# Kernel optimization log

Hardware: AMD Instinct MI355X
Metric: run time of the kernel (lower is better)

Reference implementation:

```python
import jax, jax.numpy as jnp
import numpy as np
from math import factorial

# irreps as (mul, l, parity): hidden = 64x0e + 32x1o + 16x2e (dim 240), edge = 1x0e + 1x1o (dim 4)
HIDDEN = [(64, 0, 1), (32, 1, -1), (16, 2, 1)]
EDGE = [(1, 0, 1), (1, 1, -1)]
N_LAYERS = 6
N_NODES = 10000
N_EDGES = 160000
N_GRAPHS = 64
IN_DIM = 3
LATENT = 128  # config.LATENT_DIM_GNN
W_STD = 0.1   # weight scale keeps 6 residual bilinear layers numerically stable

def _dim(ir):
    return sum(m * (2 * l + 1) for m, l, _ in ir)

def _slices(ir):
    out, o = [], 0
    for m, l, _ in ir:
        d = m * (2 * l + 1)
        out.append(slice(o, o + d))
        o += d
    return out

def _cg(j1, m1, j2, m2, j3, m3):
    # Condon-Shortley Clebsch-Gordan <j1 m1 j2 m2 | j3 m3> (Racah formula)
    if m1 + m2 != m3:
        return 0.0
    f = lambda n: float(factorial(n))
    pre = ((2 * j3 + 1) * f(j3 + j1 - j2) * f(j3 - j1 + j2) * f(j1 + j2 - j3) / f(j1 + j2 + j3 + 1)) ** 0.5
    pre *= (f(j3 + m3) * f(j3 - m3) * f(j1 - m1) * f(j1 + m1) * f(j2 - m2) * f(j2 + m2)) ** 0.5
    s = 0.0
    for k in range(j1 + j2 - j3 + 1):
        a = [k, j1 + j2 - j3 - k, j1 - m1 - k, j2 + m2 - k, j3 - j2 + m1 + k, j3 - j1 - m2 + k]
        if any(t < 0 for t in a):
            continue
        s += (-1) ** k / np.prod([f(t) for t in a])
    return pre * s

def _w3j_complex(l1, l2, l3):
    W = np.zeros((2 * l1 + 1, 2 * l2 + 1, 2 * l3 + 1))
    for m1 in range(-l1, l1 + 1):
        for m2 in range(-l2, l2 + 1):
            m3 = -(m1 + m2)
            if abs(m3) > l3:
                continue
            W[m1 + l1, m2 + l2, m3 + l3] = (-1) ** (l1 - l2 - m3) / np.sqrt(2 * l3 + 1) * _cg(l1, m1, l2, m2, l3, -m3)
    return W

def _A_real(l):
    # real SH in terms of complex SH: Y^r_m = sum_mu A[m, mu] Y_mu
    A = np.zeros((2 * l + 1, 2 * l + 1), dtype=complex)
    A[l, l] = 1.0
    for m in range(1, l + 1):
        A[l + m, l + m] = (-1) ** m / np.sqrt(2)
        A[l + m, l - m] = 1 / np.sqrt(2)
        A[l - m, l + m] = -1j * (-1) ** m / np.sqrt(2)
        A[l - m, l - m] = 1j / np.sqrt(2)
    return A

_W3J_CACHE = {}
def real_w3j(l1, l2, l3):
    key = (l1, l2, l3)
    if key not in _W3J_CACHE:
        T = np.einsum('ad,be,cf,def->abc', _A_real(l1), _A_real(l2), _A_real(l3), _w3j_complex(l1, l2, l3).astype(complex))
        T = np.real(T)  # exactly real when l1+l2+l3 is even (true for all paths here)
        _W3J_CACHE[key] = (T / np.linalg.norm(T)).astype(np.float32)
    return _W3J_CACHE[key]

def _paths(ir1, ir2, irout):
    ps = []
    for i1, (_, l1, p1) in enumerate(ir1):
        for i2, (_, l2, p2) in enumerate(ir2):
            for i3, (_, l3, p3) in enumerate(irout):
                if p3 == p1 * p2 and abs(l1 - l2) <= l3 <= l1 + l2:
                    ps.append((i1, i2, i3))
    return ps

MSG_PATHS = _paths(HIDDEN, EDGE, HIDDEN)
UPD_PATHS = _paths(HIDDEN, HIDDEN, HIDDEN)

def _tp_wsize(ir1, ir2, irout, paths):
    return sum(ir1[a][0] * ir2[b][0] * irout[c][0] for a, b, c in paths)

MSG_WSIZE = _tp_wsize(HIDDEN, EDGE, HIDDEN, MSG_PATHS)
UPD_WSIZE = _tp_wsize(HIDDEN, HIDDEN, HIDDEN, UPD_PATHS)
LIN_WSIZE = sum(m * m for m, _, _ in HIDDEN)

def tensor_product(x1, x2, w_flat, ir1, ir2, irout, paths):
    # FullyConnectedTensorProduct: per-path CG-coupled bilinear op with path normalization
    s1, s2, s3 = _slices(ir1), _slices(ir2), _slices(irout)
    npo = [0] * len(irout)
    for _, _, i3 in paths:
        npo[i3] += 1
    out = jnp.zeros((x1.shape[0], _dim(irout)), dtype=x1.dtype)
    off = 0
    for i1, i2, i3 in paths:
        m1, l1, _ = ir1[i1]; m2, l2, _ = ir2[i2]; m3, l3, _ = irout[i3]
        W = w_flat[off:off + m1 * m2 * m3].reshape(m1, m2, m3)
        off += m1 * m2 * m3
        C = jnp.asarray(real_w3j(l1, l2, l3), dtype=x1.dtype)
        a = x1[:, s1[i1]].reshape(-1, m1, 2 * l1 + 1)
        b = x2[:, s2[i2]].reshape(-1, m2, 2 * l2 + 1)
        alpha = 1.0 / np.sqrt(m1 * m2 * npo[i3])
        y = alpha * jnp.einsum('nui,nvj,uvw,ijk->nwk', a, b, W, C)
        out = out.at[:, s3[i3]].add(y.reshape(-1, m3 * (2 * l3 + 1)))
    return out

def irreps_linear(x, w_flat, ir):
    # e3nn Linear with identical in/out irreps: per-irrep mixing of multiplicities
    sl = _slices(ir)
    parts, off = [], 0
    for i, (m, l, _) in enumerate(ir):
        W = w_flat[off:off + m * m].reshape(m, m)
        off += m * m
        xi = x[:, sl[i]].reshape(-1, m, 2 * l + 1)
        parts.append((jnp.einsum('nui,uv->nvi', xi, W) / np.sqrt(m)).reshape(-1, m * (2 * l + 1)))
    return jnp.concatenate(parts, axis=-1)

def _forward(x, pos, w_init, w_tp_msg, w_lin_msg, w_tp_upd, w_lin_upd, w_final, edge_index, batch):
    row, col = edge_index[0], edge_index[1]
    r_vec = pos[row] - pos[col]                           # (E, 3)
    dist = jnp.linalg.norm(r_vec, axis=-1, keepdims=True)
    nvec = r_vec / jnp.maximum(dist, 1e-8)
    edge_attr = jnp.concatenate([dist, nvec], axis=-1)    # layer consumes [dist, r_vec] = 1x0e + 1x1o
    h = jnp.zeros((x.shape[0], _dim(HIDDEN)), dtype=x.dtype)
    h = h.at[:, :64].set(x @ w_init / np.sqrt(IN_DIM))    # initial Linear hits only 0e channels
    for L in range(N_LAYERS):
        hj = h[col]  # gather neighbor (source) features
        msg = tensor_product(hj, edge_attr, w_tp_msg[L], HIDDEN, EDGE, HIDDEN, MSG_PATHS) \
            + irreps_linear(hj, w_lin_msg[L], HIDDEN)
        agg = jax.ops.segment_sum(msg, row, num_segments=N_NODES)  # scatter-add aggregate
        upd = tensor_product(h, agg, w_tp_upd[L], HIDDEN, HIDDEN, HIDDEN, UPD_PATHS) \
            + irreps_linear(h, w_lin_upd[L], HIDDEN)
        h = h + upd  # residual
    scal = h[:, :64]  # 0e (invariant) channels
    cnt = jax.ops.segment_sum(jnp.ones((x.shape[0],), x.dtype), batch, num_segments=N_GRAPHS)
    pooled = jax.ops.segment_sum(scal, batch, num_segments=N_GRAPHS) / jnp.maximum(cnt, 1.0)[:, None]
    return pooled @ w_final / np.sqrt(64)

def setup_inputs() -> dict:
    key = jax.random.key(0)
    ks = jax.random.split(key, 10)
    return {
        'x': jax.random.normal(ks[0], (N_NODES, IN_DIM), jnp.float32),
        'pos': jax.random.normal(ks[1], (N_NODES, 3), jnp.float32),
        'w_init': jax.random.normal(ks[2], (IN_DIM, 64), jnp.float32),
        'w_tp_msg': jax.random.normal(ks[3], (N_LAYERS, MSG_WSIZE), jnp.float32) * W_STD,
        'w_lin_msg': jax.random.normal(ks[4], (N_LAYERS, LIN_WSIZE), jnp.float32) * W_STD,
        'w_tp_upd': jax.random.normal(ks[5], (N_LAYERS, UPD_WSIZE), jnp.float32) * W_STD,
        'w_lin_upd': jax.random.normal(ks[6], (N_LAYERS, LIN_WSIZE), jnp.float32) * W_STD,
        'w_final': jax.random.normal(ks[7], (64, LATENT), jnp.float32),
        'edge_index': jax.random.randint(ks[8], (2, N_EDGES), 0, N_NODES),
        'batch': jnp.sort(jax.random.randint(ks[9], (N_NODES,), 0, N_GRAPHS)),
    }

def reference(x, pos, w_init, w_tp_msg, w_lin_msg, w_tp_upd, w_lin_upd, w_final, edge_index, batch):
    return _forward(x, pos, w_init, w_tp_msg, w_lin_msg, w_tp_upd, w_lin_upd, w_final, edge_index, batch)
```

## Files before the change

kernel.cpp:

```cpp
#include <hip/hip_runtime.h>
#include <cmath>
#include <cstring>
#include <complex>

#define NN 10000
#define NE 160000
#define HD 240
#define ZD 912
#define NG 64
#define MSG_WS 10496
#define UPD_WS 561152
#define LIN_WS 5376

struct CMsgPre { float a000, a011, a110, a112, a211; float c101[9]; float c202[25]; };
struct CEdge   { float c011[9]; float c110[9]; float c112[45]; float c211[45]; };
struct CUpdS   { float s000; float c011[9]; float c022[25]; float c101[9]; float c202[25]; };
struct CUpdD   { float c110[9]; float c220[25]; };
struct CUpdP   { float c112[45]; float c121[45]; float c211[45]; float c222[125]; };


__global__ __launch_bounds__(256) void k_edge_attr(
    const float* __restrict__ pos, const int* __restrict__ ei, CEdge C,
    float* __restrict__ EA, float* __restrict__ CN) {
  int e = blockIdx.x * 256 + threadIdx.x;
  if (e >= NE) return;
  int r = ei[e], c = ei[NE + e];
  float dx = pos[r*3+0] - pos[c*3+0];
  float dy = pos[r*3+1] - pos[c*3+1];
  float dz = pos[r*3+2] - pos[c*3+2];
  float d = sqrtf(dx*dx + dy*dy + dz*dz);
  float inv = 1.0f / fmaxf(d, 1e-8f);
  float n0 = dx*inv, n1 = dy*inv, n2 = dz*inv;
  EA[e*4+0] = d; EA[e*4+1] = n0; EA[e*4+2] = n1; EA[e*4+3] = n2;
  float* cn = CN + (size_t)e*36;
#pragma unroll
  for (int k = 0; k < 3; k++)
    cn[k] = n0*C.c011[0*3+k] + n1*C.c011[1*3+k] + n2*C.c011[2*3+k];
#pragma unroll
  for (int i = 0; i < 3; i++)
    cn[3+i] = n0*C.c110[i*3+0] + n1*C.c110[i*3+1] + n2*C.c110[i*3+2];
#pragma unroll
  for (int i = 0; i < 3; i++)
#pragma unroll
    for (int k = 0; k < 5; k++)
      cn[6+i*5+k] = n0*C.c112[(i*3+0)*5+k] + n1*C.c112[(i*3+1)*5+k] + n2*C.c112[(i*3+2)*5+k];
#pragma unroll
  for (int i = 0; i < 5; i++)
#pragma unroll
    for (int k = 0; k < 3; k++)
      cn[21+i*3+k] = n0*C.c211[(i*3+0)*3+k] + n1*C.c211[(i*3+1)*3+k] + n2*C.c211[(i*3+2)*3+k];
}

__global__ __launch_bounds__(256) void k_h_init(
    const float* __restrict__ x, const float* __restrict__ wi, float* __restrict__ HT) {
  int n = blockIdx.x * 256 + threadIdx.x;
  int e = blockIdx.y;
  if (n >= NN) return;
  float v = 0.f;
  if (e < 64)
    v = (x[n*3+0]*wi[0*64+e] + x[n*3+1]*wi[64+e] + x[n*3+2]*wi[128+e]) * 0.57735026918962576f;
  HT[e*NN + n] = v;
}

__global__ __launch_bounds__(256) void k_node_pre(
    const float* __restrict__ HT, const float* __restrict__ Wm, const float* __restrict__ Wl,
    CMsgPre C, float* __restrict__ Z) {
  int n = blockIdx.x * 256 + threadIdx.x;
  int widx = blockIdx.y;
  if (n >= NN) return;
  float acc = 0.f;
  if (widx < 64) {
    int w = widx;
    for (int u = 0; u < 64; u++) acc += HT[u*NN+n] * Wm[u*64+w];
    acc *= C.a000;
  } else if (widx < 96) {
    int w = widx - 64;
    for (int u = 0; u < 64; u++) acc += HT[u*NN+n] * Wm[4096 + u*32+w];
    acc *= C.a011;
  } else if (widx < 192) {
    int t = widx - 96, w = t/3, k = t - w*3;
    for (int u = 0; u < 32; u++) {
      float g = HT[(64+u*3+0)*NN+n]*C.c101[0*3+k]
              + HT[(64+u*3+1)*NN+n]*C.c101[1*3+k]
              + HT[(64+u*3+2)*NN+n]*C.c101[2*3+k];
      acc += Wm[6144 + u*32+w] * g;
    }
  } else if (widx < 384) {
    int t = widx - 192, w = t/3, i = t - w*3;
    for (int u = 0; u < 32; u++) acc += HT[(64+u*3+i)*NN+n] * Wm[7168 + u*64+w];
    acc *= C.a110;
  } else if (widx < 432) {
    int t = widx - 384, w = t/3, i = t - w*3;
    for (int u = 0; u < 32; u++) acc += HT[(64+u*3+i)*NN+n] * Wm[9216 + u*16+w];
    acc *= C.a112;
  } else if (widx < 512) {
    int t = widx - 432, w = t/5, k = t - w*5;
    for (int u = 0; u < 16; u++) {
      float g = 0.f;
#pragma unroll
      for (int i = 0; i < 5; i++) g += HT[(160+u*5+i)*NN+n] * C.c202[i*5+k];
      acc += Wm[9728 + u*16+w] * g;
    }
  } else if (widx < 672) {
    int t = widx - 512, w = t/5, i = t - w*5;
    for (int u = 0; u < 16; u++) acc += HT[(160+u*5+i)*NN+n] * Wm[9984 + u*32+w];
    acc *= C.a211;
  } else {
    int e2 = widx - 672;
    if (e2 < 64) {
      for (int u = 0; u < 64; u++) acc += HT[u*NN+n] * Wl[u*64+e2];
      acc *= 0.125f;
    } else if (e2 < 160) {
      int t = e2 - 64, v = t/3, i = t - v*3;
      for (int u = 0; u < 32; u++) acc += HT[(64+u*3+i)*NN+n] * Wl[4096 + u*32+v];
      acc *= 0.17677669529663687f;
    } else {
      int t = e2 - 160, v = t/5, i = t - v*5;
      for (int u = 0; u < 16; u++) acc += HT[(160+u*5+i)*NN+n] * Wl[5120 + u*16+v];
      acc *= 0.25f;
    }
  }
  Z[(size_t)n*ZD + widx] = acc;
}

__global__ __launch_bounds__(256) void k_edge(
    const int* __restrict__ ei, const float* __restrict__ EA, const float* __restrict__ CN,
    const float* __restrict__ Z, float* __restrict__ AGG) {
  __shared__ float zsh[4][ZD];
  int lane = threadIdx.x & 63, wid = threadIdx.x >> 6;
  int wg = blockIdx.x * 4 + wid;
  int stride = gridDim.x * 4;
  int iters = (NE + stride - 1) / stride;
  for (int it = 0; it < iters; ++it) {
    int e = wg + it * stride;
    bool act = e < NE;
    int r = 0;
    float s = 0.f;
    const float* cn = CN;
    if (act) {
      r = ei[e];
      int c = ei[NE + e];
      s = EA[e*4];
      cn = CN + (size_t)e*36;
      const float* zr = Z + (size_t)c*ZD;
      for (int t = lane; t < ZD; t += 64) zsh[wid][t] = zr[t];
    }
    __syncthreads();
    if (act) {
      const float* z = zsh[wid];
#pragma unroll
      for (int j = 0; j < 4; j++) {
        int idx = lane + 64*j;
        if (idx < HD) {
          float y = z[672 + idx];
          if (idx < 64) {
            int w = idx;
            y += s * z[w];
#pragma unroll
            for (int i = 0; i < 3; i++) y += z[192 + w*3 + i] * cn[3+i];
          } else if (idx < 160) {
            int t = idx - 64, w = t/3, k = t - w*3;
            y += cn[k] * z[64 + w] + s * z[96 + t];
#pragma unroll
            for (int i = 0; i < 5; i++) y += z[512 + w*5 + i] * cn[21 + i*3 + k];
          } else {
            int t = idx - 160, w = t/5, k = t - w*5;
            y += s * z[432 + t];
#pragma unroll
            for (int i = 0; i < 3; i++) y += z[384 + w*3 + i] * cn[6 + i*5 + k];
          }
          atomicAdd(&AGG[(size_t)r*HD + idx], y);
        }
      }
    }
    __syncthreads();
  }
}

__global__ __launch_bounds__(256) void k_transpose(
    const float* __restrict__ A_nm, float* __restrict__ A_t) {
  int n = blockIdx.x * 256 + threadIdx.x;
  int e = blockIdx.y;
  if (n >= NN) return;
  A_t[e*NN + n] = A_nm[(size_t)n*HD + e];
}

__global__ __launch_bounds__(256) void k_upd(
    const float* __restrict__ A,
    const float* __restrict__ B,
    const float* __restrict__ W,
    CUpdS CS, CUpdD CD, CUpdP CP,
    float* __restrict__ UPD) {
  __shared__ float lds[4096];
  int tid = threadIdx.x;
  int n = blockIdx.x * 256 + tid;
  bool act = n < NN;
  int nc = act ? n : NN - 1;
  int py = blockIdx.y;

  if (py < 4) {
    int w0 = py * 16;
    float y[16];
#pragma unroll
    for (int w = 0; w < 16; w++) y[w] = 0.f;

    for (int c = 0; c < 16; ++c) {
      __syncthreads();
      for (int t = tid; t < 4096; t += 256) {
        int u2 = t >> 10, v = (t >> 4) & 63, w = t & 15;
        lds[t] = W[(((c << 2) + u2) * 64 + v) * 64 + w0 + w];
      }
      __syncthreads();
      float ha[4];
#pragma unroll
      for (int u2 = 0; u2 < 4; u2++) ha[u2] = A[((c << 2) + u2) * NN + nc] * CS.s000;
#pragma unroll 2
      for (int v = 0; v < 64; ++v) {
        float bv = B[v * NN + nc];
#pragma unroll
        for (int u2 = 0; u2 < 4; u2++) {
          float p = ha[u2] * bv;
          const float* wl = lds + (u2 << 10) + (v << 4);
#pragma unroll
          for (int w = 0; w < 16; w++) y[w] += p * wl[w];
        }
      }
    }

    for (int c = 0; c < 4; ++c) {
      __syncthreads();
      for (int t = tid; t < 4096; t += 256) {
        int u2 = t >> 9, v = (t >> 4) & 31, w = t & 15;
        lds[t] = W[409600 + ((c * 8 + u2) * 32 + v) * 64 + w0 + w];
      }
      __syncthreads();
      float a[8][3];
#pragma unroll
      for (int u2 = 0; u2 < 8; u2++)
#pragma unroll
        for (int i = 0; i < 3; i++) a[u2][i] = A[(64 + (c * 8 + u2) * 3 + i) * NN + nc];
#pragma unroll 2
      for (int v = 0; v < 32; ++v) {
        float b0 = B[(64 + v * 3 + 0) * NN + nc], b1 = B[(64 + v * 3 + 1) * NN + nc],
              b2 = B[(64 + v * 3 + 2) * NN + nc];
        float bt[3];
#pragma unroll
        for (int i = 0; i < 3; i++)
          bt[i] = CD.c110[i * 3 + 0] * b0 + CD.c110[i * 3 + 1] * b1 + CD.c110[i * 3 + 2] * b2;
#pragma unroll
        for (int u2 = 0; u2 < 8; u2++) {
          float D = a[u2][0] * bt[0] + a[u2][1] * bt[1] + a[u2][2] * bt[2];
          const float* wl = lds + u2 * 512 + v * 16;
#pragma unroll
          for (int w = 0; w < 16; w++) y[w] += D * wl[w];
        }
      }
    }

    __syncthreads();
    for (int t = tid; t < 4096; t += 256) {
      int u = t >> 8, v = (t >> 4) & 15, w = t & 15;
      lds[t] = W[540672 + (u * 16 + v) * 64 + w0 + w];
    }
    __syncthreads();
    for (int ug = 0; ug < 2; ++ug) {
      float a[8][5];
#pragma unroll
      for (int u2 = 0; u2 < 8; u2++)
#pragma unroll
        for (int i = 0; i < 5; i++) a[u2][i] = A[(160 + (ug * 8 + u2) * 5 + i) * NN + nc];
      for (int v = 0; v < 16; ++v) {
        float b[5];
#pragma unroll
        for (int j = 0; j < 5; j++) b[j] = B[(160 + v * 5 + j) * NN + nc];
        float bt[5];
#pragma unroll
        for (int i = 0; i < 5; i++) {
          float t2 = 0.f;
#pragma unroll
          for (int j = 0; j < 5; j++) t2 += CD.c220[i * 5 + j] * b[j];
          bt[i] = t2;
        }
#pragma unroll
        for (int u2 = 0; u2 < 8; u2++) {
          float D = 0.f;
#pragma unroll
          for (int i = 0; i < 5; i++) D += a[u2][i] * bt[i];
          const float* wl = lds + (ug * 8 + u2) * 256 + v * 16;
#pragma unroll
          for (int w = 0; w < 16; w++) y[w] += D * wl[w];
        }
      }
    }

    if (act) {
#pragma unroll
      for (int w = 0; w < 16; w++) UPD[(w0 + w) * NN + nc] = y[w];
    }

  } else if (py < 8) {
    int w0 = (py - 4) * 8;
    float y[24];
#pragma unroll
    for (int q = 0; q < 24; q++) y[q] = 0.f;

    for (int c = 0; c < 4; ++c) {
      __syncthreads();
      for (int t = tid; t < 4096; t += 256) {
        int u2 = t >> 8, v = (t >> 3) & 31, w = t & 7;
        lds[t] = W[262144 + ((c * 16 + u2) * 32 + v) * 32 + w0 + w];
      }
      __syncthreads();
      float a[16];
#pragma unroll
      for (int u2 = 0; u2 < 16; u2++) a[u2] = A[(c * 16 + u2) * NN + nc];
#pragma unroll 2
      for (int v = 0; v < 32; ++v) {
        float b0 = B[(64 + v * 3 + 0) * NN + nc], b1 = B[(64 + v * 3 + 1) * NN + nc],
              b2 = B[(64 + v * 3 + 2) * NN + nc];
        float bc[3];
#pragma unroll
        for (int k = 0; k < 3; k++) bc[k] = b0 * CS.c011[k] + b1 * CS.c011[3 + k] + b2 * CS.c011[6 + k];
        float g8[8];
#pragma unroll
        for (int w = 0; w < 8; w++) g8[w] = 0.f;
#pragma unroll
        for (int u2 = 0; u2 < 16; u2++) {
          const float* wl = lds + u2 * 256 + v * 8;
#pragma unroll
          for (int w = 0; w < 8; w++) g8[w] += a[u2] * wl[w];
        }
#pragma unroll
        for (int w = 0; w < 8; w++)
#pragma unroll
          for (int k = 0; k < 3; k++) y[w * 3 + k] += bc[k] * g8[w];
      }
    }

    for (int c = 0; c < 4; ++c) {
      __syncthreads();
      for (int t = tid; t < 4096; t += 256) {
        int u2 = t >> 9, v = (t >> 3) & 63, w = t & 7;
        lds[t] = W[344064 + ((c * 8 + u2) * 64 + v) * 32 + w0 + w];
      }
      __syncthreads();
      float ac[8][3];
#pragma unroll
      for (int u2 = 0; u2 < 8; u2++) {
        float a0 = A[(64 + (c * 8 + u2) * 3 + 0) * NN + nc];
        float a1 = A[(64 + (c * 8 + u2) * 3 + 1) * NN + nc];
        float a2 = A[(64 + (c * 8 + u2) * 3 + 2) * NN + nc];
#pragma unroll
        for (int k = 0; k < 3; k++)
          ac[u2][k] = a0 * CS.c101[k] + a1 * CS.c101[3 + k] + a2 * CS.c101[6 + k];
      }
      float g[8][8];
#pragma unroll
      for (int u2 = 0; u2 < 8; u2++)
#pragma unroll
        for (int w = 0; w < 8; w++) g[u2][w] = 0.f;
#pragma unroll 2
      for (int v = 0; v < 64; ++v) {
        float bv = B[v * NN + nc];
#pragma unroll
        for (int u2 = 0; u2 < 8; u2++) {
          const float* wl = lds + u2 * 512 + v * 8;
#pragma unroll
          for (int w = 0; w < 8; w++) g[u2][w] += bv * wl[w];
        }
      }
#pragma unroll
      for (int u2 = 0; u2 < 8; u2++)
#pragma unroll
        for (int w = 0; w < 8; w++)
#pragma unroll
          for (int k = 0; k < 3; k++) y[w * 3 + k] += ac[u2][k] * g[u2][w];
    }

    __syncthreads();
    for (int t = tid; t < 4096; t += 256) {
      int u = t >> 7, v = (t >> 3) & 15, w = t & 7;
      lds[t] = W[491520 + (u * 16 + v) * 32 + w0 + w];
    }
    __syncthreads();
    for (int ug = 0; ug < 4; ++ug) {
      float a[8][3];
#pragma unroll
      for (int u2 = 0; u2 < 8; u2++)
#pragma unroll
        for (int i = 0; i < 3; i++) a[u2][i] = A[(64 + (ug * 8 + u2) * 3 + i) * NN + nc];
      for (int v = 0; v < 16; ++v) {
        float b[5];
#pragma unroll
        for (int j = 0; j < 5; j++) b[j] = B[(160 + v * 5 + j) * NN + nc];
        float bt[9];
#pragma unroll
        for (int i = 0; i < 3; i++)
#pragma unroll
          for (int k = 0; k < 3; k++) {
            float t2 = 0.f;
#pragma unroll
            for (int j = 0; j < 5; j++) t2 += b[j] * CP.c121[(i * 5 + j) * 3 + k];
            bt[i * 3 + k] = t2;
          }
#pragma unroll
        for (int u2 = 0; u2 < 8; u2++) {
          float P[3];
#pragma unroll
          for (int k = 0; k < 3; k++)
            P[k] = a[u2][0] * bt[k] + a[u2][1] * bt[3 + k] + a[u2][2] * bt[6 + k];
          const float* wl = lds + (ug * 8 + u2) * 128 + v * 8;
#pragma unroll
          for (int w = 0; w < 8; w++)
#pragma unroll
            for (int k = 0; k < 3; k++) y[w * 3 + k] += P[k] * wl[w];
        }
      }
    }

    __syncthreads();
    for (int t = tid; t < 4096; t += 256) {
      int u = t >> 8, v = (t >> 3) & 31, w = t & 7;
      lds[t] = W[524288 + (u * 32 + v) * 32 + w0 + w];
    }
    __syncthreads();
    for (int ug = 0; ug < 2; ++ug) {
      float a[8][5];
#pragma unroll
      for (int u2 = 0; u2 < 8; u2++)
#pragma unroll
        for (int i = 0; i < 5; i++) a[u2][i] = A[(160 + (ug * 8 + u2) * 5 + i) * NN + nc];
#pragma unroll 2
      for (int v = 0; v < 32; ++v) {
        float b0 = B[(64 + v * 3 + 0) * NN + nc], b1 = B[(64 + v * 3 + 1) * NN + nc],
              b2 = B[(64 + v * 3 + 2) * NN + nc];
        float bt[15];
#pragma unroll
        for (int i = 0; i < 5; i++)
#pragma unroll
          for (int k = 0; k < 3; k++)
            bt[i * 3 + k] = b0 * CP.c211[(i * 3 + 0) * 3 + k] + b1 * CP.c211[(i * 3 + 1) * 3 + k] +
                            b2 * CP.c211[(i * 3 + 2) * 3 + k];
#pragma unroll
        for (int u2 = 0; u2 < 8; u2++) {
          float P[3];
#pragma unroll
          for (int k = 0; k < 3; k++) {
            float t2 = 0.f;
#pragma unroll
            for (int i = 0; i < 5; i++) t2 += a[u2][i] * bt[i * 3 + k];
            P[k] = t2;
          }
          const float* wl = lds + (ug * 8 + u2) * 256 + v * 8;
#pragma unroll
          for (int w = 0; w < 8; w++)
#pragma unroll
            for (int k = 0; k < 3; k++) y[w * 3 + k] += P[k] * wl[w];
        }
      }
    }

    if (act) {
#pragma unroll
      for (int w = 0; w < 8; w++)
#pragma unroll
        for (int k = 0; k < 3; k++) UPD[(64 + (w0 + w) * 3 + k) * NN + nc] = y[w * 3 + k];
    }

  } else {
    int w0 = (py - 8) * 4;
    float y[20];
#pragma unroll
    for (int q = 0; q < 20; q++) y[q] = 0.f;

    __syncthreads();
    for (int t = tid; t < 4096; t += 256) {
      int u = t >> 6, v = (t >> 2) & 15, w = t & 3;
      lds[t] = W[327680 + (u * 16 + v) * 16 + w0 + w];
    }
    __syncthreads();
    for (int ug = 0; ug < 4; ++ug) {
      float a[16];
#pragma unroll
      for (int u2 = 0; u2 < 16; u2++) a[u2] = A[(ug * 16 + u2) * NN + nc];
      for (int v = 0; v < 16; ++v) {
        float b[5];
#pragma unroll
        for (int j = 0; j < 5; j++) b[j] = B[(160 + v * 5 + j) * NN + nc];
        float bc[5];
#pragma unroll
        for (int k = 0; k < 5; k++) {
          float t2 = 0.f;
#pragma unroll
          for (int j = 0; j < 5; j++) t2 += b[j] * CS.c022[j * 5 + k];
          bc[k] = t2;
        }
        float g4[4];
#pragma unroll
        for (int w = 0; w < 4; w++) g4[w] = 0.f;
#pragma unroll
        for (int u2 = 0; u2 < 16; u2++) {
          const float* wl = lds + (ug * 16 + u2) * 64 + v * 4;
#pragma unroll
          for (int w = 0; w < 4; w++) g4[w] += a[u2] * wl[w];
        }
#pragma unroll
        for (int w = 0; w < 4; w++)
#pragma unroll
          for (int k = 0; k < 5; k++) y[w * 5 + k] += bc[k] * g4[w];
      }
    }

    __syncthreads();
    for (int t = tid; t < 4096; t += 256) {
      int u = t >> 8, v = (t >> 2) & 63, w = t & 3;
      lds[t] = W[507904 + (u * 64 + v) * 16 + w0 + w];
    }
    __syncthreads();
    for (int ug = 0; ug < 2; ++ug) {
      float ac[8][5];
#pragma unroll
      for (int u2 = 0; u2 < 8; u2++) {
        float a[5];
#pragma unroll
        for (int i = 0; i < 5; i++) a[i] = A[(160 + (ug * 8 + u2) * 5 + i) * NN + nc];
#pragma unroll
        for (int k = 0; k < 5; k++) {
          float t2 = 0.f;
#pragma unroll
          for (int i = 0; i < 5; i++) t2 += a[i] * CS.c202[i * 5 + k];
          ac[u2][k] = t2;
        }
      }
      float g[8][4];
#pragma unroll
      for (int u2 = 0; u2 < 8; u2++)
#pragma unroll
        for (int w = 0; w < 4; w++) g[u2][w] = 0.f;
#pragma unroll 2
      for (int v = 0; v < 64; ++v) {
        float bv = B[v * NN + nc];
#pragma unroll
        for (int u2 = 0; u2 < 8; u2++) {
          const float* wl = lds + (ug * 8 + u2) * 256 + v * 4;
#pragma unroll
          for (int w = 0; w < 4; w++) g[u2][w] += bv * wl[w];
        }
      }
#pragma unroll
      for (int u2 = 0; u2 < 8; u2++)
#pragma unroll
        for (int w = 0; w < 4; w++)
#pragma unroll
          for (int k = 0; k < 5; k++) y[w * 5 + k] += ac[u2][k] * g[u2][w];
    }

    __syncthreads();
    for (int t = tid; t < 4096; t += 256) {
      int u = t >> 7, v = (t >> 2) & 31, w = t & 3;
      lds[t] = W[475136 + (u * 32 + v) * 16 + w0 + w];
    }
    __syncthreads();
    for (int ug = 0; ug < 4; ++ug) {
      float a[8][3];
#pragma unroll
      for (int u2 = 0; u2 < 8; u2++)
#pragma unroll
        for (int i = 0; i < 3; i++) a[u2][i] = A[(64 + (ug * 8 + u2) * 3 + i) * NN + nc];
#pragma unroll 2
      for (int v = 0; v < 32; ++v) {
        float b0 = B[(64 + v * 3 + 0) * NN + nc], b1 = B[(64 + v * 3 + 1) * NN + nc],
              b2 = B[(64 + v * 3 + 2) * NN + nc];
        float bt[15];
#pragma unroll
        for (int i = 0; i < 3; i++)
#pragma unroll
          for (int k = 0; k < 5; k++)
            bt[i * 5 + k] = b0 * CP.c112[(i * 3 + 0) * 5 + k] + b1 * CP.c112[(i * 3 + 1) * 5 + k] +
                            b2 * CP.c112[(i * 3 + 2) * 5 + k];
#pragma unroll
        for (int u2 = 0; u2 < 8; u2++) {
          float P[5];
#pragma unroll
          for (int k = 0; k < 5; k++)
            P[k] = a[u2][0] * bt[k] + a[u2][1] * bt[5 + k] + a[u2][2] * bt[10 + k];
          const float* wl = lds + ((ug * 8 + u2) * 32 + v) * 4;
#pragma unroll
          for (int w = 0; w < 4; w++)
#pragma unroll
            for (int k = 0; k < 5; k++) y[w * 5 + k] += P[k] * wl[w];
        }
      }
    }

    __syncthreads();
    for (int t = tid; t < 1024; t += 256) {
      int u = t >> 6, v = (t >> 2) & 15, w = t & 3;
      lds[t] = W[557056 + (u * 16 + v) * 16 + w0 + w];
    }
    __syncthreads();
    for (int ug = 0; ug < 2; ++ug) {
      float a[8][5];
#pragma unroll
      for (int u2 = 0; u2 < 8; u2++)
#pragma unroll
        for (int i = 0; i < 5; i++) a[u2][i] = A[(160 + (ug * 8 + u2) * 5 + i) * NN + nc];
      for (int v = 0; v < 16; ++v) {
        float b[5];
#pragma unroll
        for (int j = 0; j < 5; j++) b[j] = B[(160 + v * 5 + j) * NN + nc];
        float bt[25];
#pragma unroll
        for (int i = 0; i < 5; i++)
#pragma unroll
          for (int k = 0; k < 5; k++) {
            float t2 = 0.f;
#pragma unroll
            for (int j = 0; j < 5; j++) t2 += b[j] * CP.c222[(i * 5 + j) * 5 + k];
            bt[i * 5 + k] = t2;
          }
#pragma unroll
        for (int u2 = 0; u2 < 8; u2++) {
          float P[5];
#pragma unroll
          for (int k = 0; k < 5; k++) {
            float t2 = 0.f;
#pragma unroll
            for (int i = 0; i < 5; i++) t2 += a[u2][i] * bt[i * 5 + k];
            P[k] = t2;
          }
          const float* wl = lds + (ug * 8 + u2) * 64 + v * 4;
#pragma unroll
          for (int w = 0; w < 4; w++)
#pragma unroll
            for (int k = 0; k < 5; k++) y[w * 5 + k] += P[k] * wl[w];
        }
      }
    }

    if (act) {
#pragma unroll
      for (int w = 0; w < 4; w++)
#pragma unroll
        for (int k = 0; k < 5; k++) UPD[(160 + (w0 + w) * 5 + k) * NN + nc] = y[w * 5 + k];
    }
  }
}

__global__ __launch_bounds__(256) void k_apply(
    const float* __restrict__ Hsrc, const float* __restrict__ UPD,
    const float* __restrict__ Wl, float* __restrict__ Hdst) {
  int n = blockIdx.x * 256 + threadIdx.x;
  int e = blockIdx.y;
  if (n >= NN) return;
  float lin = 0.f;
  if (e < 64) {
    for (int u = 0; u < 64; u++) lin += Hsrc[u*NN+n] * Wl[u*64+e];
    lin *= 0.125f;
  } else if (e < 160) {
    int t = e - 64, v = t/3, i = t - v*3;
    for (int u = 0; u < 32; u++) lin += Hsrc[(64+u*3+i)*NN+n] * Wl[4096 + u*32+v];
    lin *= 0.17677669529663687f;
  } else {
    int t = e - 160, v = t/5, i = t - v*5;
    for (int u = 0; u < 16; u++) lin += Hsrc[(160+u*5+i)*NN+n] * Wl[5120 + u*16+v];
    lin *= 0.25f;
  }
  Hdst[e*NN + n] = Hsrc[e*NN + n] + UPD[e*NN + n] + lin;
}

__global__ __launch_bounds__(256) void k_cnt(const int* __restrict__ batch, float* __restrict__ CNT) {
  int n = blockIdx.x * 256 + threadIdx.x;
  if (n >= NN) return;
  atomicAdd(&CNT[batch[n]], 1.0f);
}

__global__ __launch_bounds__(256) void k_pool(
    const float* __restrict__ HT, const int* __restrict__ batch, float* __restrict__ POOL) {
  int n = blockIdx.x * 256 + threadIdx.x;
  int w = blockIdx.y;
  if (n >= NN) return;
  atomicAdd(&POOL[batch[n]*64 + w], HT[w*NN + n]);
}

__global__ __launch_bounds__(256) void k_out(
    const float* __restrict__ POOL, const float* __restrict__ CNT,
    const float* __restrict__ wf, float* __restrict__ out) {
  int tid = blockIdx.x * 256 + threadIdx.x;
  if (tid >= NG * 128) return;
  int g = tid >> 7, d = tid & 127;
  float inv = 1.0f / fmaxf(CNT[g], 1.0f);
  float acc = 0.f;
  for (int w = 0; w < 64; w++) acc += POOL[g*64 + w] * wf[w*128 + d];
  out[tid] = acc * inv * 0.125f;
}

typedef std::complex<double> cd;
static double hfact(int nn) { double f = 1; for (int i = 2; i <= nn; i++) f *= i; return f; }
static double hcg(int j1,int m1,int j2,int m2,int j3,int m3) {
  if (m1 + m2 != m3) return 0.0;
  double pre = sqrt((2*j3+1) * hfact(j3+j1-j2) * hfact(j3-j1+j2) * hfact(j1+j2-j3) / hfact(j1+j2+j3+1));
  pre *= sqrt(hfact(j3+m3)*hfact(j3-m3)*hfact(j1-m1)*hfact(j1+m1)*hfact(j2-m2)*hfact(j2+m2));
  double s = 0;
  for (int k = 0; k <= j1+j2-j3; k++) {
    int a1=j1+j2-j3-k, a2=j1-m1-k, a3=j2+m2-k, a4=j3-j2+m1+k, a5=j3-j1-m2+k;
    if (a1<0||a2<0||a3<0||a4<0||a5<0) continue;
    s += ((k&1)?-1.0:1.0) / (hfact(k)*hfact(a1)*hfact(a2)*hfact(a3)*hfact(a4)*hfact(a5));
  }
  return pre * s;
}
static void hA(int l, cd A[5][5]) {
  for (int r = 0; r < 5; r++) for (int c = 0; c < 5; c++) A[r][c] = cd(0,0);
  A[l][l] = cd(1,0);
  for (int m = 1; m <= l; m++) {
    double sg = (m & 1) ? -1.0 : 1.0;
    A[l+m][l+m] = cd(sg/sqrt(2.0), 0);
    A[l+m][l-m] = cd(1.0/sqrt(2.0), 0);
    A[l-m][l+m] = cd(0, -sg/sqrt(2.0));
    A[l-m][l-m] = cd(0, 1.0/sqrt(2.0));
  }
}
static void hw3j(int l1, int l2, int l3, double* out) {
  int n1 = 2*l1+1, n2 = 2*l2+1, n3 = 2*l3+1;
  double Wc[5][5][5]; memset(Wc, 0, sizeof Wc);
  for (int m1 = -l1; m1 <= l1; m1++) for (int m2 = -l2; m2 <= l2; m2++) {
    int m3 = -(m1+m2);
    if (m3 < -l3 || m3 > l3) continue;
    int ex = l1 - l2 - m3;
    double sg = (ex % 2 == 0) ? 1.0 : -1.0;
    Wc[m1+l1][m2+l2][m3+l3] = sg / sqrt((double)(2*l3+1)) * hcg(l1,m1,l2,m2,l3,-m3);
  }
  cd A1[5][5], A2[5][5], A3[5][5];
  hA(l1,A1); hA(l2,A2); hA(l3,A3);
  double nrm = 0;
  for (int a = 0; a < n1; a++) for (int b = 0; b < n2; b++) for (int c = 0; c < n3; c++) {
    cd acc(0,0);
    for (int d = 0; d < n1; d++) for (int e = 0; e < n2; e++) for (int f = 0; f < n3; f++) {
      double w = Wc[d][e][f];
      if (w == 0.0) continue;
      acc += A1[a][d] * A2[b][e] * A3[c][f] * w;
    }
    out[(a*n2+b)*n3+c] = acc.real();
    nrm += acc.real() * acc.real();
  }
  nrm = sqrt(nrm);
  for (int i = 0; i < n1*n2*n3; i++) out[i] /= nrm;
}

extern "C" void kernel_launch(void* const* d_in, const int* in_sizes, int n_in,
                              void* d_out, int out_size, void* d_ws, size_t ws_size,
                              hipStream_t stream) {
  const float* x        = (const float*)d_in[0];
  const float* pos      = (const float*)d_in[1];
  const float* w_init   = (const float*)d_in[2];
  const float* w_tp_msg = (const float*)d_in[3];
  const float* w_lin_msg= (const float*)d_in[4];
  const float* w_tp_upd = (const float*)d_in[5];
  const float* w_lin_upd= (const float*)d_in[6];
  const float* w_final  = (const float*)d_in[7];
  const int*   ei       = (const int*)d_in[8];
  const int*   batch    = (const int*)d_in[9];
  float* out = (float*)d_out;
  float* ws  = (float*)d_ws;

  float* EA     = ws;
  float* CN     = EA + 640000;
  float* HTA    = CN + 5760000;
  float* HTB    = HTA + 2400000;
  float* Z      = HTB + 2400000;
  float* AGG_NM = Z + 9120000;
  float* UPD_T  = AGG_NM + 2400000;
  float* AGG_T  = UPD_T + 2400000;
  float* POOL   = AGG_T + 2400000;
  float* CNT    = POOL + 4096;

  double C000d[1], C011d[9], C101d[9], C110d[9], C112d[45], C022d[25],
         C202d[25], C121d[45], C211d[45], C220d[25], C222d[125];
  hw3j(0,0,0,C000d); hw3j(0,1,1,C011d); hw3j(1,0,1,C101d); hw3j(1,1,0,C110d);
  hw3j(1,1,2,C112d); hw3j(0,2,2,C022d); hw3j(2,0,2,C202d); hw3j(1,2,1,C121d);
  hw3j(2,1,1,C211d); hw3j(2,2,0,C220d); hw3j(2,2,2,C222d);

  CMsgPre cmsg;
  cmsg.a000 = (float)(C000d[0] / sqrt(128.0));
  cmsg.a011 = (float)(1.0 / sqrt(192.0));
  cmsg.a110 = (float)(1.0 / sqrt(64.0));
  cmsg.a112 = (float)(1.0 / sqrt(64.0));
  cmsg.a211 = (float)(1.0 / sqrt(48.0));
  for (int i = 0; i < 9;  i++) cmsg.c101[i] = (float)(C101d[i] / sqrt(96.0));
  for (int i = 0; i < 25; i++) cmsg.c202[i] = (float)(C202d[i] / sqrt(32.0));

  CEdge ce;
  for (int i = 0; i < 9;  i++) ce.c011[i] = (float)C011d[i];
  for (int i = 0; i < 9;  i++) ce.c110[i] = (float)C110d[i];
  for (int i = 0; i < 45; i++) ce.c112[i] = (float)C112d[i];
  for (int i = 0; i < 45; i++) ce.c211[i] = (float)C211d[i];

  CUpdS cus;
  cus.s000 = (float)(C000d[0] / sqrt(64.0*64.0*3.0));
  for (int i = 0; i < 9;  i++) cus.c011[i] = (float)(C011d[i] / sqrt(64.0*32.0*4.0));
  for (int i = 0; i < 25; i++) cus.c022[i] = (float)(C022d[i] / sqrt(64.0*16.0*4.0));
  for (int i = 0; i < 9;  i++) cus.c101[i] = (float)(C101d[i] / sqrt(32.0*64.0*4.0));
  for (int i = 0; i < 25; i++) cus.c202[i] = (float)(C202d[i] / sqrt(16.0*64.0*4.0));

  CUpdD cud;
  for (int i = 0; i < 9;  i++) cud.c110[i] = (float)(C110d[i] / sqrt(32.0*32.0*3.0));
  for (int i = 0; i < 25; i++) cud.c220[i] = (float)(C220d[i] / sqrt(16.0*16.0*3.0));

  CUpdP cup;
  for (int i = 0; i < 45;  i++) cup.c112[i] = (float)(C112d[i] / sqrt(32.0*32.0*4.0));
  for (int i = 0; i < 45;  i++) cup.c121[i] = (float)(C121d[i] / sqrt(32.0*16.0*4.0));
  for (int i = 0; i < 45;  i++) cup.c211[i] = (float)(C211d[i] / sqrt(16.0*32.0*4.0));
  for (int i = 0; i < 125; i++) cup.c222[i] = (float)(C222d[i] / sqrt(16.0*16.0*4.0));

  k_edge_attr<<<(NE+255)/256, 256, 0, stream>>>(pos, ei, ce, EA, CN);
  k_h_init<<<dim3(40, HD), 256, 0, stream>>>(x, w_init, HTA);

  float* cur = HTA;
  float* nxt = HTB;
  for (int L = 0; L < 6; L++) {
    hipMemsetAsync(AGG_NM, 0, (size_t)2400000 * sizeof(float), stream);
    k_node_pre<<<dim3(40, ZD), 256, 0, stream>>>(cur, w_tp_msg + (size_t)L*MSG_WS,
                                                 w_lin_msg + (size_t)L*LIN_WS, cmsg, Z);
    k_edge<<<1280, 256, 0, stream>>>(ei, EA, CN, Z, AGG_NM);
    k_transpose<<<dim3(40, HD), 256, 0, stream>>>(AGG_NM, AGG_T);
    const float* Wu = w_tp_upd + (size_t)L*UPD_WS;
    k_upd<<<dim3(40, 12), 256, 0, stream>>>(cur, AGG_T, Wu, cus, cud, cup, UPD_T);
    k_apply<<<dim3(40, HD), 256, 0, stream>>>(cur, UPD_T, w_lin_upd + (size_t)L*LIN_WS, nxt);
    float* tmp = cur; cur = nxt; nxt = tmp;
  }

  hipMemsetAsync(POOL, 0, (size_t)(4096 + 64) * sizeof(float), stream);
  k_cnt<<<(NN+255)/256, 256, 0, stream>>>(batch, CNT);
  k_pool<<<dim3(40, 64), 256, 0, stream>>>(cur, batch, POOL);
  k_out<<<32, 256, 0, stream>>>(POOL, CNT, w_final, out);
}
```

Before: 5.521 ms.

## Retile node update kernel: two nodes per thread, four outputs per block, float4 LDS weights

```diff
diff --git a/kernel.cpp b/kernel.cpp
--- a/kernel.cpp
+++ b/kernel.cpp
@@ -185,466 +185,517 @@
   A_t[e*NN + n] = A_nm[(size_t)n*HD + e];
 }
 
-__global__ __launch_bounds__(256) void k_upd(
+__global__ __launch_bounds__(128, 2) void k_upd(
     const float* __restrict__ A,
     const float* __restrict__ B,
     const float* __restrict__ W,
     CUpdS CS, CUpdD CD, CUpdP CP,
     float* __restrict__ UPD) {
-  __shared__ float lds[4096];
-  int tid = threadIdx.x;
-  int n = blockIdx.x * 256 + tid;
-  bool act = n < NN;
-  int nc = act ? n : NN - 1;
-  int py = blockIdx.y;
-
-  if (py < 4) {
-    int w0 = py * 16;
-    float y[16];
-#pragma unroll
-    for (int w = 0; w < 16; w++) y[w] = 0.f;
-
-    for (int c = 0; c < 16; ++c) {
-      __syncthreads();
-      for (int t = tid; t < 4096; t += 256) {
-        int u2 = t >> 10, v = (t >> 4) & 63, w = t & 15;
-        lds[t] = W[(((c << 2) + u2) * 64 + v) * 64 + w0 + w];
-      }
-      __syncthreads();
-      float ha[4];
-#pragma unroll
-      for (int u2 = 0; u2 < 4; u2++) ha[u2] = A[((c << 2) + u2) * NN + nc] * CS.s000;
-#pragma unroll 2
-      for (int v = 0; v < 64; ++v) {
-        float bv = B[v * NN + nc];
-#pragma unroll
-        for (int u2 = 0; u2 < 4; u2++) {
-          float p = ha[u2] * bv;
-          const float* wl = lds + (u2 << 10) + (v << 4);
-#pragma unroll
-          for (int w = 0; w < 16; w++) y[w] += p * wl[w];
-        }
-      }
-    }
-
-    for (int c = 0; c < 4; ++c) {
-      __syncthreads();
-      for (int t = tid; t < 4096; t += 256) {
-        int u2 = t >> 9, v = (t >> 4) & 31, w = t & 15;
-        lds[t] = W[409600 + ((c * 8 + u2) * 32 + v) * 64 + w0 + w];
-      }
-      __syncthreads();
-      float a[8][3];
-#pragma unroll
-      for (int u2 = 0; u2 < 8; u2++)
-#pragma unroll
-        for (int i = 0; i < 3; i++) a[u2][i] = A[(64 + (c * 8 + u2) * 3 + i) * NN + nc];
-#pragma unroll 2
-      for (int v = 0; v < 32; ++v) {
-        float b0 = B[(64 + v * 3 + 0) * NN + nc], b1 = B[(64 + v * 3 + 1) * NN + nc],
-              b2 = B[(64 + v * 3 + 2) * NN + nc];
-        float bt[3];
-#pragma unroll
-        for (int i = 0; i < 3; i++)
-          bt[i] = CD.c110[i * 3 + 0] * b0 + CD.c110[i * 3 + 1] * b1 + CD.c110[i * 3 + 2] * b2;
-#pragma unroll
-        for (int u2 = 0; u2 < 8; u2++) {
-          float D = a[u2][0] * bt[0] + a[u2][1] * bt[1] + a[u2][2] * bt[2];
-          const float* wl = lds + u2 * 512 + v * 16;
-#pragma unroll
-          for (int w = 0; w < 16; w++) y[w] += D * wl[w];
-        }
-      }
-    }
-
-    __syncthreads();
-    for (int t = tid; t < 4096; t += 256) {
-      int u = t >> 8, v = (t >> 4) & 15, w = t & 15;
-      lds[t] = W[540672 + (u * 16 + v) * 64 + w0 + w];
-    }
-    __syncthreads();
-    for (int ug = 0; ug < 2; ++ug) {
-      float a[8][5];
-#pragma unroll
-      for (int u2 = 0; u2 < 8; u2++)
-#pragma unroll
-        for (int i = 0; i < 5; i++) a[u2][i] = A[(160 + (ug * 8 + u2) * 5 + i) * NN + nc];
+  __shared__ float4 lds4[1024];
+  const int tid = threadIdx.x;
+  const int n0 = blockIdx.x * 256 + tid;
+  const int n1 = n0 + 128;
+  const bool ok0 = n0 < NN, ok1 = n1 < NN;
+  const int nc0 = ok0 ? n0 : NN - 1;
+  const int nc1 = ok1 ? n1 : NN - 1;
+  const int py = blockIdx.y;
+
+#define LDA2(dst, e) { int _e=(e); dst.x = A[_e*NN+nc0]; dst.y = A[_e*NN+nc1]; }
+#define LDB2(dst, e) { int _e=(e); dst.x = B[_e*NN+nc0]; dst.y = B[_e*NN+nc1]; }
+
+  if (py < 16) {
+    const int w04 = py;
+    float2 y[4];
+#pragma unroll
+    for (int w = 0; w < 4; w++) y[w] = make_float2(0.f, 0.f);
+
+    {
+      const float4* W4 = (const float4*)W;
+      for (int uc = 0; uc < 4; ++uc) {
+        __syncthreads();
+        for (int t = tid; t < 1024; t += 128) lds4[t] = W4[(uc*1024 + t)*16 + w04];
+        __syncthreads();
+        float2 ha[16];
+#pragma unroll
+        for (int u = 0; u < 16; ++u) {
+          LDA2(ha[u], uc*16 + u);
+          ha[u].x *= CS.s000; ha[u].y *= CS.s000;
+        }
+        for (int v = 0; v < 64; ++v) {
+          float2 bv; LDB2(bv, v);
+#pragma unroll
+          for (int u = 0; u < 16; ++u) {
+            float4 wl = lds4[u*64 + v];
+            float px = ha[u].x * bv.x, qx = ha[u].y * bv.y;
+            y[0].x += px*wl.x; y[0].y += qx*wl.x;
+            y[1].x += px*wl.y; y[1].y += qx*wl.y;
+            y[2].x += px*wl.z; y[2].y += qx*wl.z;
+            y[3].x += px*wl.w; y[3].y += qx*wl.w;
+          }
+        }
+      }
+    }
+
+    {
+      const float4* W4 = (const float4*)(W + 409600);
+      __syncthreads();
+      for (int t = tid; t < 1024; t += 128) lds4[t] = W4[t*16 + w04];
+      __syncthreads();
+      for (int uc = 0; uc < 4; ++uc) {
+        float2 a[8][3];
+#pragma unroll
+        for (int u = 0; u < 8; ++u)
+#pragma unroll
+          for (int i = 0; i < 3; ++i) LDA2(a[u][i], 64 + (uc*8+u)*3 + i);
+        for (int v = 0; v < 32; ++v) {
+          float2 b[3];
+#pragma unroll
+          for (int j = 0; j < 3; ++j) LDB2(b[j], 64 + v*3 + j);
+          float2 bt[3];
+#pragma unroll
+          for (int i = 0; i < 3; ++i) {
+            bt[i].x = CD.c110[i*3+0]*b[0].x + CD.c110[i*3+1]*b[1].x + CD.c110[i*3+2]*b[2].x;
+            bt[i].y = CD.c110[i*3+0]*b[0].y + CD.c110[i*3+1]*b[1].y + CD.c110[i*3+2]*b[2].y;
+          }
+#pragma unroll
+          for (int u = 0; u < 8; ++u) {
+            float Dx = a[u][0].x*bt[0].x + a[u][1].x*bt[1].x + a[u][2].x*bt[2].x;
+            float Dy = a[u][0].y*bt[0].y + a[u][1].y*bt[1].y + a[u][2].y*bt[2].y;
+            float4 wl = lds4[(uc*8+u)*32 + v];
+            y[0].x += Dx*wl.x; y[0].y += Dy*wl.x;
+            y[1].x += Dx*wl.y; y[1].y += Dy*wl.y;
+            y[2].x += Dx*wl.z; y[2].y += Dy*wl.z;
+            y[3].x += Dx*wl.w; y[3].y += Dy*wl.w;
+          }
+        }
+      }
+    }
+
+    {
+      const float4* W4 = (const float4*)(W + 540672);
+      __syncthreads();
+      for (int t = tid; t < 256; t += 128) lds4[t] = W4[t*16 + w04];
+      __syncthreads();
+      for (int uc = 0; uc < 4; ++uc) {
+        float2 a[4][5];
+#pragma unroll
+        for (int u = 0; u < 4; ++u)
+#pragma unroll
+          for (int i = 0; i < 5; ++i) LDA2(a[u][i], 160 + (uc*4+u)*5 + i);
+        for (int v = 0; v < 16; ++v) {
+          float2 b[5];
+#pragma unroll
+          for (int j = 0; j < 5; ++j) LDB2(b[j], 160 + v*5 + j);
+          float2 bt[5];
+#pragma unroll
+          for (int i = 0; i < 5; ++i) {
+            float tx = 0.f, ty = 0.f;
+#pragma unroll
+            for (int j = 0; j < 5; ++j) { tx += CD.c220[i*5+j]*b[j].x; ty += CD.c220[i*5+j]*b[j].y; }
+            bt[i].x = tx; bt[i].y = ty;
+          }
+#pragma unroll
+          for (int u = 0; u < 4; ++u) {
+            float Dx = 0.f, Dy = 0.f;
+#pragma unroll
+            for (int i = 0; i < 5; ++i) { Dx += a[u][i].x*bt[i].x; Dy += a[u][i].y*bt[i].y; }
+            float4 wl = lds4[(uc*4+u)*16 + v];
+            y[0].x += Dx*wl.x; y[0].y += Dy*wl.x;
+            y[1].x += Dx*wl.y; y[1].y += Dy*wl.y;
+            y[2].x += Dx*wl.z; y[2].y += Dy*wl.z;
+            y[3].x += Dx*wl.w; y[3].y += Dy*wl.w;
+          }
+        }
+      }
+    }
+
+#pragma unroll
+    for (int w = 0; w < 4; ++w) {
+      if (ok0) UPD[(py*4 + w)*NN + n0] = y[w].x;
+      if (ok1) UPD[(py*4 + w)*NN + n1] = y[w].y;
+    }
+
+  } else if (py < 24) {
+    const int w04 = py - 16;
+    float2 y[4][3];
+#pragma unroll
+    for (int w = 0; w < 4; w++)
+#pragma unroll
+      for (int k = 0; k < 3; k++) y[w][k] = make_float2(0.f, 0.f);
+
+    {
+      const float4* W4 = (const float4*)(W + 262144);
+      for (int uc = 0; uc < 2; ++uc) {
+        __syncthreads();
+        for (int t = tid; t < 1024; t += 128) lds4[t] = W4[(uc*1024 + t)*8 + w04];
+        __syncthreads();
+        float2 a[32];
+#pragma unroll
+        for (int u = 0; u < 32; ++u) LDA2(a[u], uc*32 + u);
+        for (int v = 0; v < 32; ++v) {
+          float2 b[3];
+#pragma unroll
+          for (int j = 0; j < 3; ++j) LDB2(b[j], 64 + v*3 + j);
+          float2 bc[3];
+#pragma unroll
+          for (int k = 0; k < 3; ++k) {
+            bc[k].x = b[0].x*CS.c011[k] + b[1].x*CS.c011[3+k] + b[2].x*CS.c011[6+k];
+            bc[k].y = b[0].y*CS.c011[k] + b[1].y*CS.c011[3+k] + b[2].y*CS.c011[6+k];
+          }
+          float2 g[4];
+#pragma unroll
+          for (int w = 0; w < 4; w++) g[w] = make_float2(0.f, 0.f);
+#pragma unroll
+          for (int u = 0; u < 32; ++u) {
+            float4 wl = lds4[u*32 + v];
+            g[0].x += a[u].x*wl.x; g[0].y += a[u].y*wl.x;
+            g[1].x += a[u].x*wl.y; g[1].y += a[u].y*wl.y;
+            g[2].x += a[u].x*wl.z; g[2].y += a[u].y*wl.z;
+            g[3].x += a[u].x*wl.w; g[3].y += a[u].y*wl.w;
+          }
+#pragma unroll
+          for (int w = 0; w < 4; ++w)
+#pragma unroll
+            for (int k = 0; k < 3; ++k) {
+              y[w][k].x += bc[k].x*g[w].x; y[w][k].y += bc[k].y*g[w].y;
+            }
+        }
+      }
+    }
+
+    {
+      const float4* W4 = (const float4*)(W + 344064);
+      for (int uc = 0; uc < 2; ++uc) {
+        __syncthreads();
+        for (int t = tid; t < 1024; t += 128) lds4[t] = W4[(uc*1024 + t)*8 + w04];
+        __syncthreads();
+        for (int vc = 0; vc < 4; ++vc) {
+          float2 bv[16];
+#pragma unroll
+          for (int v2 = 0; v2 < 16; ++v2) LDB2(bv[v2], vc*16 + v2);
+          for (int u = 0; u < 16; ++u) {
+            float2 aa[3];
+#pragma unroll
+            for (int i = 0; i < 3; ++i) LDA2(aa[i], 64 + (uc*16+u)*3 + i);
+            float2 ac[3];
+#pragma unroll
+            for (int k = 0; k < 3; ++k) {
+              ac[k].x = aa[0].x*CS.c101[k] + aa[1].x*CS.c101[3+k] + aa[2].x*CS.c101[6+k];
+              ac[k].y = aa[0].y*CS.c101[k] + aa[1].y*CS.c101[3+k] + aa[2].y*CS.c101[6+k];
+            }
+            float2 gp[4];
+#pragma unroll
+            for (int w = 0; w < 4; w++) gp[w] = make_float2(0.f, 0.f);
+#pragma unroll
+            for (int v2 = 0; v2 < 16; ++v2) {
+              float4 wl = lds4[u*64 + vc*16 + v2];
+              gp[0].x += bv[v2].x*wl.x; gp[0].y += bv[v2].y*wl.x;
+              gp[1].x += bv[v2].x*wl.y; gp[1].y += bv[v2].y*wl.y;
+              gp[2].x += bv[v2].x*wl.z; gp[2].y += bv[v2].y*wl.z;
+              gp[3].x += bv[v2].x*wl.w; gp[3].y += bv[v2].y*wl.w;
+            }
+#pragma unroll
+            for (int w = 0; w < 4; ++w)
+#pragma unroll
+              for (int k = 0; k < 3; ++k) {
+                y[w][k].x += ac[k].x*gp[w].x; y[w][k].y += ac[k].y*gp[w].y;
+              }
+          }
+        }
+      }
+    }
+
+    {
+      const float4* W4 = (const float4*)(W + 491520);
+      __syncthreads();
+      for (int t = tid; t < 512; t += 128) lds4[t] = W4[t*8 + w04];
+      __syncthreads();
+      for (int uc = 0; uc < 4; ++uc) {
+        float2 a[8][3];
+#pragma unroll
+        for (int u = 0; u < 8; ++u)
+#pragma unroll
+          for (int i = 0; i < 3; ++i) LDA2(a[u][i], 64 + (uc*8+u)*3 + i);
+        for (int v = 0; v < 16; ++v) {
+          float2 b[5];
+#pragma unroll
+          for (int j = 0; j < 5; ++j) LDB2(b[j], 160 + v*5 + j);
+          float2 bt[3][3];
+#pragma unroll
+          for (int i = 0; i < 3; ++i)
+#pragma unroll
+            for (int k = 0; k < 3; ++k) {
+              float tx = 0.f, ty = 0.f;
+#pragma unroll
+              for (int j = 0; j < 5; ++j) { tx += b[j].x*CP.c121[(i*5+j)*3+k]; ty += b[j].y*CP.c121[(i*5+j)*3+k]; }
+              bt[i][k].x = tx; bt[i][k].y = ty;
+            }
+#pragma unroll
+          for (int u = 0; u < 8; ++u) {
+            float2 P[3];
+#pragma unroll
+            for (int k = 0; k < 3; ++k) {
+              P[k].x = a[u][0].x*bt[0][k].x + a[u][1].x*bt[1][k].x + a[u][2].x*bt[2][k].x;
+              P[k].y = a[u][0].y*bt[0][k].y + a[u][1].y*bt[1][k].y + a[u][2].y*bt[2][k].y;
+            }
+            float4 wl = lds4[(uc*8+u)*16 + v];
+#pragma unroll
+            for (int k = 0; k < 3; ++k) {
+              y[0][k].x += P[k].x*wl.x; y[0][k].y += P[k].y*wl.x;
+              y[1][k].x += P[k].x*wl.y; y[1][k].y += P[k].y*wl.y;
+              y[2][k].x += P[k].x*wl.z; y[2][k].y += P[k].y*wl.z;
+              y[3][k].x += P[k].x*wl.w; y[3][k].y += P[k].y*wl.w;
+            }
+          }
+        }
+      }
+    }
+
+    {
+      const float4* W4 = (const float4*)(W + 524288);
+      __syncthreads();
+      for (int t = tid; t < 512; t += 128) lds4[t] = W4[t*8 + w04];
+      __syncthreads();
+      for (int uc = 0; uc < 2; ++uc) {
+        float2 a[8][5];
+#pragma unroll
+        for (int u = 0; u < 8; ++u)
+#pragma unroll
+          for (int i = 0; i < 5; ++i) LDA2(a[u][i], 160 + (uc*8+u)*5 + i);
+        for (int v = 0; v < 32; ++v) {
+          float2 b[3];
+#pragma unroll
+          for (int j = 0; j < 3; ++j) LDB2(b[j], 64 + v*3 + j);
+          float2 bt[5][3];
+#pragma unroll
+          for (int i = 0; i < 5; ++i)
+#pragma unroll
+            for (int k = 0; k < 3; ++k) {
+              bt[i][k].x = b[0].x*CP.c211[(i*3+0)*3+k] + b[1].x*CP.c211[(i*3+1)*3+k] + b[2].x*CP.c211[(i*3+2)*3+k];
+              bt[i][k].y = b[0].y*CP.c211[(i*3+0)*3+k] + b[1].y*CP.c211[(i*3+1)*3+k] + b[2].y*CP.c211[(i*3+2)*3+k];
+            }
+#pragma unroll
+          for (int u = 0; u < 8; ++u) {
+            float2 P[3];
+#pragma unroll
+            for (int k = 0; k < 3; ++k) {
+              float tx = 0.f, ty = 0.f;
+#pragma unroll
+              for (int i = 0; i < 5; ++i) { tx += a[u][i].x*bt[i][k].x; ty += a[u][i].y*bt[i][k].y; }
+              P[k].x = tx; P[k].y = ty;
+            }
+            float4 wl = lds4[(uc*8+u)*32 + v];
+#pragma unroll
+            for (int k = 0; k < 3; ++k) {
+              y[0][k].x += P[k].x*wl.x; y[0][k].y += P[k].y*wl.x;
+              y[1][k].x += P[k].x*wl.y; y[1][k].y += P[k].y*wl.y;
+              y[2][k].x += P[k].x*wl.z; y[2][k].y += P[k].y*wl.z;
+              y[3][k].x += P[k].x*wl.w; y[3][k].y += P[k].y*wl.w;
+            }
+          }
+        }
+      }
+    }
+
+#pragma unroll
+    for (int w = 0; w < 4; ++w)
+#pragma unroll
+      for (int k = 0; k < 3; ++k) {
+        int e = 64 + (w04*4 + w)*3 + k;
+        if (ok0) UPD[e*NN + n0] = y[w][k].x;
+        if (ok1) UPD[e*NN + n1] = y[w][k].y;
+      }
+
+  } else {
+    const int w04 = py - 24;
+    float2 y[4][5];
+#pragma unroll
+    for (int w = 0; w < 4; w++)
+#pragma unroll
+      for (int k = 0; k < 5; k++) y[w][k] = make_float2(0.f, 0.f);
+
+    {
+      const float4* W4 = (const float4*)(W + 327680);
+      __syncthreads();
+      for (int t = tid; t < 1024; t += 128) lds4[t] = W4[t*4 + w04];
+      __syncthreads();
+      for (int uc = 0; uc < 4; ++uc) {
+        float2 a[16];
+#pragma unroll
+        for (int u = 0; u < 16; ++u) LDA2(a[u], uc*16 + u);
+        for (int v = 0; v < 16; ++v) {
+          float2 b[5];
+#pragma unroll
+          for (int j = 0; j < 5; ++j) LDB2(b[j], 160 + v*5 + j);
+          float2 bc[5];
+#pragma unroll
+          for (int k = 0; k < 5; ++k) {
+            float tx = 0.f, ty = 0.f;
+#pragma unroll
+            for (int j = 0; j < 5; ++j) { tx += b[j].x*CS.c022[j*5+k]; ty += b[j].y*CS.c022[j*5+k]; }
+            bc[k].x = tx; bc[k].y = ty;
+          }
+          float2 g[4];
+#pragma unroll
+          for (int w = 0; w < 4; w++) g[w] = make_float2(0.f, 0.f);
+#pragma unroll
+          for (int u = 0; u < 16; ++u) {
+            float4 wl = lds4[(uc*16+u)*16 + v];
+            g[0].x += a[u].x*wl.x; g[0].y += a[u].y*wl.x;
+            g[1].x += a[u].x*wl.y; g[1].y += a[u].y*wl.y;
+            g[2].x += a[u].x*wl.z; g[2].y += a[u].y*wl.z;
+            g[3].x += a[u].x*wl.w; g[3].y += a[u].y*wl.w;
+          }
+#pragma unroll
+          for (int w = 0; w < 4; ++w)
+#pragma unroll
+            for (int k = 0; k < 5; ++k) {
+              y[w][k].x += bc[k].x*g[w].x; y[w][k].y += bc[k].y*g[w].y;
+            }
+        }
+      }
+    }
+
+    {
+      const float4* W4 = (const float4*)(W + 507904);
+      __syncthreads();
+      for (int t = tid; t < 1024; t += 128) lds4[t] = W4[t*4 + w04];
+      __syncthreads();
+      for (int vc = 0; vc < 4; ++vc) {
+        float2 bv[16];
+#pragma unroll
+        for (int v2 = 0; v2 < 16; ++v2) LDB2(bv[v2], vc*16 + v2);
+        for (int u = 0; u < 16; ++u) {
+          float2 aa[5];
+#pragma unroll
+          for (int i = 0; i < 5; ++i) LDA2(aa[i], 160 + u*5 + i);
+          float2 ac[5];
+#pragma unroll
+          for (int k = 0; k < 5; ++k) {
+            float tx = 0.f, ty = 0.f;
+#pragma unroll
+            for (int i = 0; i < 5; ++i) { tx += aa[i].x*CS.c202[i*5+k]; ty += aa[i].y*CS.c202[i*5+k]; }
+            ac[k].x = tx; ac[k].y = ty;
+          }
+          float2 gp[4];
+#pragma unroll
+          for (int w = 0; w < 4; w++) gp[w] = make_float2(0.f, 0.f);
+#pragma unroll
+          for (int v2 = 0; v2 < 16; ++v2) {
+            float4 wl = lds4[u*64 + vc*16 + v2];
+            gp[0].x += bv[v2].x*wl.x; gp[0].y += bv[v2].y*wl.x;
+            gp[1].x += bv[v2].x*wl.y; gp[1].y += bv[v2].y*wl.y;
+            gp[2].x += bv[v2].x*wl.z; gp[2].y += bv[v2].y*wl.z;
+            gp[3].x += bv[v2].x*wl.w; gp[3].y += bv[v2].y*wl.w;
+          }
+#pragma unroll
+          for (int w = 0; w < 4; ++w)
+#pragma unroll
+            for (int k = 0; k < 5; ++k) {
+              y[w][k].x += ac[k].x*gp[w].x; y[w][k].y += ac[k].y*gp[w].y;
+            }
+        }
+      }
+    }
+
+    {
+      const float4* W4 = (const float4*)(W + 475136);
+      __syncthreads();
+      for (int t = tid; t < 1024; t += 128) lds4[t] = W4[t*4 + w04];
+      __syncthreads();
+      for (int uc = 0; uc < 4; ++uc) {
+        float2 a[8][3];
+#pragma unroll
+        for (int u = 0; u < 8; ++u)
+#pragma unroll
+          for (int i = 0; i < 3; ++i) LDA2(a[u][i], 64 + (uc*8+u)*3 + i);
+        for (int v = 0; v < 32; ++v) {
+          float2 b[3];
+#pragma unroll
+          for (int j = 0; j < 3; ++j) LDB2(b[j], 64 + v*3 + j);
+          float2 bt[3][5];
+#pragma unroll
+          for (int i = 0; i < 3; ++i)
+#pragma unroll
+            for (int k = 0; k < 5; ++k) {
+              bt[i][k].x = b[0].x*CP.c112[(i*3+0)*5+k] + b[1].x*CP.c112[(i*3+1)*5+k] + b[2].x*CP.c112[(i*3+2)*5+k];
+              bt[i][k].y = b[0].y*CP.c112[(i*3+0)*5+k] + b[1].y*CP.c112[(i*3+1)*5+k] + b[2].y*CP.c112[(i*3+2)*5+k];
+            }
+#pragma unroll
+          for (int u = 0; u < 8; ++u) {
+            float2 P[5];
+#pragma unroll
+            for (int k = 0; k < 5; ++k) {
+              P[k].x = a[u][0].x*bt[0][k].x + a[u][1].x*bt[1][k].x + a[u][2].x*bt[2][k].x;
+              P[k].y = a[u][0].y*bt[0][k].y + a[u][1].y*bt[1][k].y + a[u][2].y*bt[2][k].y;
+            }
+            float4 wl = lds4[(uc*8+u)*32 + v];
+#pragma unroll
+            for (int k = 0; k < 5; ++k) {
+              y[0][k].x += P[k].x*wl.x; y[0][k].y += P[k].y*wl.x;
+              y[1][k].x += P[k].x*wl.y; y[1][k].y += P[k].y*wl.y;
+              y[2][k].x += P[k].x*wl.z; y[2][k].y += P[k].y*wl.z;
+              y[3][k].x += P[k].x*wl.w; y[3][k].y += P[k].y*wl.w;
+            }
+          }
+        }
+      }
+    }
+
+    {
+      const float4* W4 = (const float4*)(W + 557056);
+      __syncthreads();
+      for (int t = tid; t < 256; t += 128) lds4[t] = W4[t*4 + w04];
+      __syncthreads();
       for (int v = 0; v < 16; ++v) {
-        float b[5];
-#pragma unroll
-        for (int j = 0; j < 5; j++) b[j] = B[(160 + v * 5 + j) * NN + nc];
-        float bt[5];
-#pragma unroll
-        for (int i = 0; i < 5; i++) {
-          float t2 = 0.f;
-#pragma unroll
-          for (int j = 0; j < 5; j++) t2 += CD.c220[i * 5 + j] * b[j];
-          bt[i] = t2;
-        }
-#pragma unroll
-        for (int u2 = 0; u2 < 8; u2++) {
-          float D = 0.f;
-#pragma unroll
-          for (int i = 0; i < 5; i++) D += a[u2][i] * bt[i];
-          const float* wl = lds + (ug * 8 + u2) * 256 + v * 16;
-#pragma unroll
-          for (int w = 0; w < 16; w++) y[w] += D * wl[w];
-        }
-      }
-    }
-
-    if (act) {
-#pragma unroll
-      for (int w = 0; w < 16; w++) UPD[(w0 + w) * NN + nc] = y[w];
-    }
-
-  } else if (py < 8) {
-    int w0 = (py - 4) * 8;
-    float y[24];
-#pragma unroll
-    for (int q = 0; q < 24; q++) y[q] = 0.f;
-
-    for (int c = 0; c < 4; ++c) {
-      __syncthreads();
-      for (int t = tid; t < 4096; t += 256) {
-        int u2 = t >> 8, v = (t >> 3) & 31, w = t & 7;
-        lds[t] = W[262144 + ((c * 16 + u2) * 32 + v) * 32 + w0 + w];
-      }
-      __syncthreads();
-      float a[16];
-#pragma unroll
-      for (int u2 = 0; u2 < 16; u2++) a[u2] = A[(c * 16 + u2) * NN + nc];
-#pragma unroll 2
-      for (int v = 0; v < 32; ++v) {
-        float b0 = B[(64 + v * 3 + 0) * NN + nc], b1 = B[(64 + v * 3 + 1) * NN + nc],
-              b2 = B[(64 + v * 3 + 2) * NN + nc];
-        float bc[3];
-#pragma unroll
-        for (int k = 0; k < 3; k++) bc[k] = b0 * CS.c011[k] + b1 * CS.c011[3 + k] + b2 * CS.c011[6 + k];
-        float g8[8];
-#pragma unroll
-        for (int w = 0; w < 8; w++) g8[w] = 0.f;
-#pragma unroll
-        for (int u2 = 0; u2 < 16; u2++) {
-          const float* wl = lds + u2 * 256 + v * 8;
-#pragma unroll
-          for (int w = 0; w < 8; w++) g8[w] += a[u2] * wl[w];
-        }
-#pragma unroll
-        for (int w = 0; w < 8; w++)
-#pragma unroll
-          for (int k = 0; k < 3; k++) y[w * 3 + k] += bc[k] * g8[w];
-      }
-    }
-
-    for (int c = 0; c < 4; ++c) {
-      __syncthreads();
-      for (int t = tid; t < 4096; t += 256) {
-        int u2 = t >> 9, v = (t >> 3) & 63, w = t & 7;
-        lds[t] = W[344064 + ((c * 8 + u2) * 64 + v) * 32 + w0 + w];
-      }
-      __syncthreads();
-      float ac[8][3];
-#pragma unroll
-      for (int u2 = 0; u2 < 8; u2++) {
-        float a0 = A[(64 + (c * 8 + u2) * 3 + 0) * NN + nc];
-        float a1 = A[(64 + (c * 8 + u2) * 3 + 1) * NN + nc];
-        float a2 = A[(64 + (c * 8 + u2) * 3 + 2) * NN + nc];
-#pragma unroll
-        for (int k = 0; k < 3; k++)
-          ac[u2][k] = a0 * CS.c101[k] + a1 * CS.c101[3 + k] + a2 * CS.c101[6 + k];
-      }
-      float g[8][8];
-#pragma unroll
-      for (int u2 = 0; u2 < 8; u2++)
-#pragma unroll
-        for (int w = 0; w < 8; w++) g[u2][w] = 0.f;
-#pragma unroll 2
-      for (int v = 0; v < 64; ++v) {
-        float bv = B[v * NN + nc];
-#pragma unroll
-        for (int u2 = 0; u2 < 8; u2++) {
-          const float* wl = lds + u2 * 512 + v * 8;
-#pragma unroll
-          for (int w = 0; w < 8; w++) g[u2][w] += bv * wl[w];
-        }
-      }
-#pragma unroll
-      for (int u2 = 0; u2 < 8; u2++)
-#pragma unroll
-        for (int w = 0; w < 8; w++)
-#pragma unroll
-          for (int k = 0; k < 3; k++) y[w * 3 + k] += ac[u2][k] * g[u2][w];
-    }
-
-    __syncthreads();
-    for (int t = tid; t < 4096; t += 256) {
-      int u = t >> 7, v = (t >> 3) & 15, w = t & 7;
-      lds[t] = W[491520 + (u * 16 + v) * 32 + w0 + w];
-    }
-    __syncthreads();
-    for (int ug = 0; ug < 4; ++ug) {
-      float a[8][3];
-#pragma unroll
-      for (int u2 = 0; u2 < 8; u2++)
-#pragma unroll
-        for (int i = 0; i < 3; i++) a[u2][i] = A[(64 + (ug * 8 + u2) * 3 + i) * NN + nc];
-      for (int v = 0; v < 16; ++v) {
-        float b[5];
-#pragma unroll
-        for (int j = 0; j < 5; j++) b[j] = B[(160 + v * 5 + j) * NN + nc];
-        float bt[9];
-#pragma unroll
-        for (int i = 0; i < 3; i++)
-#pragma unroll
-          for (int k = 0; k < 3; k++) {
-            float t2 = 0.f;
-#pragma unroll
-            for (int j = 0; j < 5; j++) t2 += b[j] * CP.c121[(i * 5 + j) * 3 + k];
-            bt[i * 3 + k] = t2;
-          }
-#pragma unroll
-        for (int u2 = 0; u2 < 8; u2++) {
-          float P[3];
-#pragma unroll
-          for (int k = 0; k < 3; k++)
-            P[k] = a[u2][0] * bt[k] + a[u2][1] * bt[3 + k] + a[u2][2] * bt[6 + k];
-          const float* wl = lds + (ug * 8 + u2) * 128 + v * 8;
-#pragma unroll
-          for (int w = 0; w < 8; w++)
-#pragma unroll
-            for (int k = 0; k < 3; k++) y[w * 3 + k] += P[k] * wl[w];
-        }
-      }
-    }
-
-    __syncthreads();
-    for (int t = tid; t < 4096; t += 256) {
-      int u = t >> 8, v = (t >> 3) & 31, w = t & 7;
-      lds[t] = W[524288 + (u * 32 + v) * 32 + w0 + w];
-    }
-    __syncthreads();
-    for (int ug = 0; ug < 2; ++ug) {
-      float a[8][5];
-#pragma unroll
-      for (int u2 = 0; u2 < 8; u2++)
-#pragma unroll
-        for (int i = 0; i < 5; i++) a[u2][i] = A[(160 + (ug * 8 + u2) * 5 + i) * NN + nc];
-#pragma unroll 2
-      for (int v = 0; v < 32; ++v) {
-        float b0 = B[(64 + v * 3 + 0) * NN + nc], b1 = B[(64 + v * 3 + 1) * NN + nc],
-              b2 = B[(64 + v * 3 + 2) * NN + nc];
-        float bt[15];
-#pragma unroll
-        for (int i = 0; i < 5; i++)
-#pragma unroll
-          for (int k = 0; k < 3; k++)
-            bt[i * 3 + k] = b0 * CP.c211[(i * 3 + 0) * 3 + k] + b1 * CP.c211[(i * 3 + 1) * 3 + k] +
-                            b2 * CP.c211[(i * 3 + 2) * 3 + k];
-#pragma unroll
-        for (int u2 = 0; u2 < 8; u2++) {
-          float P[3];
-#pragma unroll
-          for (int k = 0; k < 3; k++) {
-            float t2 = 0.f;
-#pragma unroll
-            for (int i = 0; i < 5; i++) t2 += a[u2][i] * bt[i * 3 + k];
-            P[k] = t2;
-          }
-          const float* wl = lds + (ug * 8 + u2) * 256 + v * 8;
-#pragma unroll
-          for (int w = 0; w < 8; w++)
-#pragma unroll
-            for (int k = 0; k < 3; k++) y[w * 3 + k] += P[k] * wl[w];
-        }
-      }
-    }
-
-    if (act) {
-#pragma unroll
-      for (int w = 0; w < 8; w++)
-#pragma unroll
-        for (int k = 0; k < 3; k++) UPD[(64 + (w0 + w) * 3 + k) * NN + nc] = y[w * 3 + k];
-    }
-
-  } else {
-    int w0 = (py - 8) * 4;
-    float y[20];
-#pragma unroll
-    for (int q = 0; q < 20; q++) y[q] = 0.f;
-
-    __syncthreads();
-    for (int t = tid; t < 4096; t += 256) {
-      int u = t >> 6, v = (t >> 2) & 15, w = t & 3;
-      lds[t] = W[327680 + (u * 16 + v) * 16 + w0 + w];
-    }
-    __syncthreads();
-    for (int ug = 0; ug < 4; ++ug) {
-      float a[16];
-#pragma unroll
-      for (int u2 = 0; u2 < 16; u2++) a[u2] = A[(ug * 16 + u2) * NN + nc];
-      for (int v = 0; v < 16; ++v) {
-        float b[5];
-#pragma unroll
-        for (int j = 0; j < 5; j++) b[j] = B[(160 + v * 5 + j) * NN + nc];
-        float bc[5];
-#pragma unroll
-        for (int k = 0; k < 5; k++) {
-          float t2 = 0.f;
-#pragma unroll
-          for (int j = 0; j < 5; j++) t2 += b[j] * CS.c022[j * 5 + k];
-          bc[k] = t2;
-        }
-        float g4[4];
-#pragma unroll
-        for (int w = 0; w < 4; w++) g4[w] = 0.f;
-#pragma unroll
-        for (int u2 = 0; u2 < 16; u2++) {
-          const float* wl = lds + (ug * 16 + u2) * 64 + v * 4;
-#pragma unroll
-          for (int w = 0; w < 4; w++) g4[w] += a[u2] * wl[w];
-        }
-#pragma unroll
-        for (int w = 0; w < 4; w++)
-#pragma unroll
-          for (int k = 0; k < 5; k++) y[w * 5 + k] += bc[k] * g4[w];
-      }
-    }
-
-    __syncthreads();
-    for (int t = tid; t < 4096; t += 256) {
-      int u = t >> 8, v = (t >> 2) & 63, w = t & 3;
-      lds[t] = W[507904 + (u * 64 + v) * 16 + w0 + w];
-    }
-    __syncthreads();
-    for (int ug = 0; ug < 2; ++ug) {
-      float ac[8][5];
-#pragma unroll
-      for (int u2 = 0; u2 < 8; u2++) {
-        float a[5];
-#pragma unroll
-        for (int i = 0; i < 5; i++) a[i] = A[(160 + (ug * 8 + u2) * 5 + i) * NN + nc];
-#pragma unroll
-        for (int k = 0; k < 5; k++) {
-          float t2 = 0.f;
-#pragma unroll
-          for (int i = 0; i < 5; i++) t2 += a[i] * CS.c202[i * 5 + k];
-          ac[u2][k] = t2;
-        }
-      }
-      float g[8][4];
-#pragma unroll
-      for (int u2 = 0; u2 < 8; u2++)
-#pragma unroll
-        for (int w = 0; w < 4; w++) g[u2][w] = 0.f;
-#pragma unroll 2
-      for (int v = 0; v < 64; ++v) {
-        float bv = B[v * NN + nc];
-#pragma unroll
-        for (int u2 = 0; u2 < 8; u2++) {
-          const float* wl = lds + (ug * 8 + u2) * 256 + v * 4;
-#pragma unroll
-          for (int w = 0; w < 4; w++) g[u2][w] += bv * wl[w];
-        }
-      }
-#pragma unroll
-      for (int u2 = 0; u2 < 8; u2++)
-#pragma unroll
-        for (int w = 0; w < 4; w++)
-#pragma unroll
-          for (int k = 0; k < 5; k++) y[w * 5 + k] += ac[u2][k] * g[u2][w];
-    }
-
-    __syncthreads();
-    for (int t = tid; t < 4096; t += 256) {
-      int u = t >> 7, v = (t >> 2) & 31, w = t & 3;
-      lds[t] = W[475136 + (u * 32 + v) * 16 + w0 + w];
-    }
-    __syncthreads();
-    for (int ug = 0; ug < 4; ++ug) {
-      float a[8][3];
-#pragma unroll
-      for (int u2 = 0; u2 < 8; u2++)
-#pragma unroll
-        for (int i = 0; i < 3; i++) a[u2][i] = A[(64 + (ug * 8 + u2) * 3 + i) * NN + nc];
-#pragma unroll 2
-      for (int v = 0; v < 32; ++v) {
-        float b0 = B[(64 + v * 3 + 0) * NN + nc], b1 = B[(64 + v * 3 + 1) * NN + nc],
-              b2 = B[(64 + v * 3 + 2) * NN + nc];
-        float bt[15];
-#pragma unroll
-        for (int i = 0; i < 3; i++)
-#pragma unroll
-          for (int k = 0; k < 5; k++)
-            bt[i * 5 + k] = b0 * CP.c112[(i * 3 + 0) * 5 + k] + b1 * CP.c112[(i * 3 + 1) * 5 + k] +
-                            b2 * CP.c112[(i * 3 + 2) * 5 + k];
-#pragma unroll
-        for (int u2 = 0; u2 < 8; u2++) {
-          float P[5];
-#pragma unroll
-          for (int k = 0; k < 5; k++)
-            P[k] = a[u2][0] * bt[k] + a[u2][1] * bt[5 + k] + a[u2][2] * bt[10 + k];
-          const float* wl = lds + ((ug * 8 + u2) * 32 + v) * 4;
-#pragma unroll
-          for (int w = 0; w < 4; w++)
-#pragma unroll
-            for (int k = 0; k < 5; k++) y[w * 5 + k] += P[k] * wl[w];
-        }
-      }
-    }
-
-    __syncthreads();
-    for (int t = tid; t < 1024; t += 256) {
-      int u = t >> 6, v = (t >> 2) & 15, w = t & 3;
-      lds[t] = W[557056 + (u * 16 + v) * 16 + w0 + w];
-    }
-    __syncthreads();
-    for (int ug = 0; ug < 2; ++ug) {
-      float a[8][5];
-#pragma unroll
-      for (int u2 = 0; u2 < 8; u2++)
-#pragma unroll
-        for (int i = 0; i < 5; i++) a[u2][i] = A[(160 + (ug * 8 + u2) * 5 + i) * NN + nc];
-      for (int v = 0; v < 16; ++v) {
-        float b[5];
-#pragma unroll
-        for (int j = 0; j < 5; j++) b[j] = B[(160 + v * 5 + j) * NN + nc];
-        float bt[25];
-#pragma unroll
-        for (int i = 0; i < 5; i++)
-#pragma unroll
-          for (int k = 0; k < 5; k++) {
-            float t2 = 0.f;
-#pragma unroll
-            for (int j = 0; j < 5; j++) t2 += b[j] * CP.c222[(i * 5 + j) * 5 + k];
-            bt[i * 5 + k] = t2;
-          }
-#pragma unroll
-        for (int u2 = 0; u2 < 8; u2++) {
-          float P[5];
-#pragma unroll
-          for (int k = 0; k < 5; k++) {
-            float t2 = 0.f;
-#pragma unroll
-            for (int i = 0; i < 5; i++) t2 += a[u2][i] * bt[i * 5 + k];
-            P[k] = t2;
-          }
-          const float* wl = lds + (ug * 8 + u2) * 64 + v * 4;
-#pragma unroll
-          for (int w = 0; w < 4; w++)
-#pragma unroll
-            for (int k = 0; k < 5; k++) y[w * 5 + k] += P[k] * wl[w];
-        }
-      }
-    }
-
-    if (act) {
-#pragma unroll
-      for (int w = 0; w < 4; w++)
-#pragma unroll
-        for (int k = 0; k < 5; k++) UPD[(160 + (w0 + w) * 5 + k) * NN + nc] = y[w * 5 + k];
-    }
+        float2 b[5];
+#pragma unroll
+        for (int j = 0; j < 5; ++j) LDB2(b[j], 160 + v*5 + j);
+        float2 bt[5][5];
+#pragma unroll
+        for (int i = 0; i < 5; ++i)
+#pragma unroll
+          for (int k = 0; k < 5; ++k) {
+            float tx = 0.f, ty = 0.f;
+#pragma unroll
+            for (int j = 0; j < 5; ++j) { tx += b[j].x*CP.c222[(i*5+j)*5+k]; ty += b[j].y*CP.c222[(i*5+j)*5+k]; }
+            bt[i][k].x = tx; bt[i][k].y = ty;
+          }
+        for (int u = 0; u < 16; ++u) {
+          float2 aa[5];
+#pragma unroll
+          for (int i = 0; i < 5; ++i) LDA2(aa[i], 160 + u*5 + i);
+          float2 P[5];
+#pragma unroll
+          for (int k = 0; k < 5; ++k) {
+            float tx = 0.f, ty = 0.f;
+#pragma unroll
+            for (int i = 0; i < 5; ++i) { tx += aa[i].x*bt[i][k].x; ty += aa[i].y*bt[i][k].y; }
+            P[k].x = tx; P[k].y = ty;
+          }
+          float4 wl = lds4[u*16 + v];
+#pragma unroll
+          for (int k = 0; k < 5; ++k) {
+            y[0][k].x += P[k].x*wl.x; y[0][k].y += P[k].y*wl.x;
+            y[1][k].x += P[k].x*wl.y; y[1][k].y += P[k].y*wl.y;
+            y[2][k].x += P[k].x*wl.z; y[2][k].y += P[k].y*wl.z;
+            y[3][k].x += P[k].x*wl.w; y[3][k].y += P[k].y*wl.w;
+          }
+        }
+      }
+    }
+
+#pragma unroll
+    for (int w = 0; w < 4; ++w)
+#pragma unroll
+      for (int k = 0; k < 5; ++k) {
+        int e = 160 + (w04*4 + w)*5 + k;
+        if (ok0) UPD[e*NN + n0] = y[w][k].x;
+        if (ok1) UPD[e*NN + n1] = y[w][k].y;
+      }
   }
+#undef LDA2
+#undef LDB2
 }
 
 __global__ __launch_bounds__(256) void k_apply(
@@ -824,7 +875,7 @@
     k_edge<<<1280, 256, 0, stream>>>(ei, EA, CN, Z, AGG_NM);
     k_transpose<<<dim3(40, HD), 256, 0, stream>>>(AGG_NM, AGG_T);
     const float* Wu = w_tp_upd + (size_t)L*UPD_WS;
-    k_upd<<<dim3(40, 12), 256, 0, stream>>>(cur, AGG_T, Wu, cus, cud, cup, UPD_T);
+    k_upd<<<dim3(40, 28), 128, 0, stream>>>(cur, AGG_T, Wu, cus, cud, cup, UPD_T);
     k_apply<<<dim3(40, HD), 256, 0, stream>>>(cur, UPD_T, w_lin_upd + (size_t)L*LIN_WS, nxt);
     float* tmp = cur; cur = nxt; nxt = tmp;
   }
```

New measurement: 5.464 ms. About the same (-1.0%).
